# Kernel optimization log

Measured on AMD Instinct MI355X. Metric: run time of the kernel, lower is better.

Reference implementation:

```python
import jax, jax.numpy as jnp
import numpy as np

EPS = 1e-5

def _layernorm(h, g, b):
    m = jnp.mean(h, axis=-1, keepdims=True)
    v = jnp.mean((h - m) ** 2, axis=-1, keepdims=True)
    return (h - m) * jax.lax.rsqrt(v + EPS) * g + b

def setup_inputs() -> dict:
    B, N, D, H, C = 16, 4096, 1024, 512, 2
    key = jax.random.key(0)
    ks = jax.random.split(key, 16)
    def lin(k, fan_in, shape):
        return jax.random.normal(k, shape, dtype=jnp.float32) / np.sqrt(fan_in)
    return {
        "x":   jax.random.normal(ks[0], (B, N, D), dtype=jnp.float32),
        "W1":  lin(ks[1], D, (D, H)),  "b1": jnp.zeros((H,), jnp.float32),
        "g1":  jnp.ones((H,), jnp.float32), "beta1": jnp.zeros((H,), jnp.float32),
        "W2":  lin(ks[2], H, (H, H)),  "b2": jnp.zeros((H,), jnp.float32),
        "g2":  jnp.ones((H,), jnp.float32), "beta2": jnp.zeros((H,), jnp.float32),
        "Wa1": lin(ks[3], H, (H, H)),  "ba1": jnp.zeros((H,), jnp.float32),
        "wa2": lin(ks[4], H, (H, 1)),  "ba2": jnp.zeros((1,), jnp.float32),
        "Wc1": lin(ks[5], H, (H, H)),  "bc1": jnp.zeros((H,), jnp.float32),
        "Wc2": lin(ks[6], H, (H, C)),  "bc2": jnp.zeros((C,), jnp.float32),
    }

def reference(x, W1, b1, g1, beta1, W2, b2, g2, beta2,
              Wa1, ba1, wa2, ba2, Wc1, bc1, Wc2, bc2):
    # Feature extractor: Linear -> LayerNorm -> ReLU (x2); dropout is identity (eval)
    h = jax.nn.relu(_layernorm(jnp.einsum('bnd,dh->bnh', x, W1) + b1, g1, beta1))
    h = jax.nn.relu(_layernorm(jnp.einsum('bnh,hk->bnk', h, W2) + b2, g2, beta2))
    # Attention: Linear -> Tanh -> Linear(->1), softmax over instances (per bag)
    scores = jnp.tanh(jnp.einsum('bnh,hk->bnk', h, Wa1) + ba1) @ wa2 + ba2  # [B,N,1]
    attn = jax.nn.softmax(scores, axis=1)                                   # [B,N,1]
    pooled = jnp.sum(h * attn, axis=1)                                      # [B,H]
    # Classifier (no sample_source path): Linear -> ReLU -> Linear
    logits = jax.nn.relu(pooled @ Wc1 + bc1) @ Wc2 + bc2                    # [B,C]
    return logits
```

## Files before the change

### kernel.cpp

```cpp
#include <hip/hip_runtime.h>
#include <hip/hip_bf16.h>


#define MTOT   65536
#define DDIM   1024
#define HDIM   512
#define NBAG   16
#define NINST  4096

typedef __attribute__((ext_vector_type(8))) short bf16x8;
typedef __attribute__((ext_vector_type(4))) float f32x4;

__device__ __forceinline__ unsigned short f2bf(float f) {
  __hip_bfloat16 h = __float2bfloat16(f);
  unsigned short u;
  __builtin_memcpy(&u, &h, 2);
  return u;
}
__device__ __forceinline__ float bf2f(unsigned short u) {
  unsigned int x = ((unsigned int)u) << 16;
  float f;
  __builtin_memcpy(&f, &x, 4);
  return f;
}

__device__ __forceinline__ void gload16(const void* g, void* l) {
  __builtin_amdgcn_global_load_lds(
      (const __attribute__((address_space(1))) unsigned int*)g,
      (__attribute__((address_space(3))) unsigned int*)l, 16, 0, 0);
}

__device__ __forceinline__ bf16x8 pack8(float4 a, float4 b) {
  bf16x8 r;
  r[0] = (short)f2bf(a.x); r[1] = (short)f2bf(a.y);
  r[2] = (short)f2bf(a.z); r[3] = (short)f2bf(a.w);
  r[4] = (short)f2bf(b.x); r[5] = (short)f2bf(b.y);
  r[6] = (short)f2bf(b.z); r[7] = (short)f2bf(b.w);
  return r;
}

__global__ void transpose_cast(const float* __restrict__ src,
                               __hip_bfloat16* __restrict__ dst,
                               int R, int C) {
  __shared__ float t[32][33];
  const int c0 = blockIdx.x * 32, r0 = blockIdx.y * 32;
  const int tx = threadIdx.x, ty = threadIdx.y;
#pragma unroll
  for (int i = 0; i < 32; i += 8)
    t[ty + i][tx] = src[(size_t)(r0 + ty + i) * C + c0 + tx];
  __syncthreads();
#pragma unroll
  for (int i = 0; i < 32; i += 8)
    dst[(size_t)(c0 + ty + i) * R + r0 + tx] = __float2bfloat16(t[tx][ty + i]);
}

#define BM 128
#define BN 128
#define BK 32

template <int KD, bool AF32, int MODE>
__global__ __launch_bounds__(256, AF32 ? 2 : 3)
void gemm_tile(const void* Ap, const __hip_bfloat16* __restrict__ BT,
               const float* __restrict__ bias,
               __hip_bfloat16* __restrict__ ybuf,
               float2* __restrict__ statp,
               const float* __restrict__ wa2,
               float* __restrict__ scorep) {
  __shared__ __align__(16) char smem[16384];
  __hip_bfloat16* AtP = (__hip_bfloat16*)smem;
  __hip_bfloat16* BtP = (__hip_bfloat16*)(smem + 8192);

  const int tid  = threadIdx.x;
  const int lane = tid & 63;
  const int w    = tid >> 6;
  const int wm   = w >> 1;
  const int wn   = w & 1;
  const int l16  = lane & 15;
  const int lg   = lane >> 4;

  const int cpx = gridDim.x >> 3;
  int bid = blockIdx.x;
  bid = (bid & 7) * cpx + (bid >> 3);
  const int n_blk   = bid & 3;
  const int row_blk = bid >> 2;
  const size_t row0 = (size_t)row_blk * BM;
  const int col0    = n_blk * BN;

  const int rS   = lane & 15;
  const int sS   = (lane >> 4) ^ (lane & 3);
  const int dOff = lane * 8;
  const int frag_off = l16 * 8 + ((lg ^ (l16 & 3)) << 7);

  constexpr int NT = KD / BK;
  const __hip_bfloat16* Abf = (const __hip_bfloat16*)Ap;
  const float* Af32 = (const float*)Ap;

  f32x4 acc[4][4];
#pragma unroll
  for (int i = 0; i < 4; i++)
#pragma unroll
    for (int j = 0; j < 4; j++) acc[i][j] = (f32x4){0.f, 0.f, 0.f, 0.f};

  auto stageB = [&](int kb) {
#pragma unroll
    for (int i = 0; i < 2; i++) {
      const int c = w * 2 + i;
      gload16(BT + (size_t)(col0 + c * 16 + rS) * KD + kb + sS * 8,
              BtP + c * 512 + dOff);
    }
  };
  auto stageA_g = [&](int kb) {
#pragma unroll
    for (int i = 0; i < 2; i++) {
      const int c = w * 2 + i;
      gload16(Abf + (row0 + c * 16 + rS) * KD + kb + sS * 8,
              AtP + c * 512 + dOff);
    }
  };

  float4 f0_0a, f0_0b, f0_1a, f0_1b, f1_0a, f1_0b, f1_1a, f1_1b;
#define LOADA_(S, KB)                                                          \
  { const float* g0_ = Af32 + (row0 + (w * 2 + 0) * 16 + rS) * KD + (KB) + sS * 8; \
    const float* g1_ = Af32 + (row0 + (w * 2 + 1) * 16 + rS) * KD + (KB) + sS * 8; \
    f##S##_0a = *(const float4*)g0_; f##S##_0b = *(const float4*)(g0_ + 4);    \
    f##S##_1a = *(const float4*)g1_; f##S##_1b = *(const float4*)(g1_ + 4); }
#define WRITEA_(S)                                                             \
  { *reinterpret_cast<bf16x8*>(AtP + (w * 2 + 0) * 512 + dOff) =               \
        pack8(f##S##_0a, f##S##_0b);                                           \
    *reinterpret_cast<bf16x8*>(AtP + (w * 2 + 1) * 512 + dOff) =               \
        pack8(f##S##_1a, f##S##_1b); }

#define FRAGS_DECL                                                             \
  bf16x8 af[4], bfr[4];                                                        \
  _Pragma("unroll") for (int fm = 0; fm < 4; fm++)                             \
      af[fm] = *reinterpret_cast<const bf16x8*>(                               \
          AtP + (wm * 4 + fm) * 512 + frag_off);                               \
  _Pragma("unroll") for (int fn = 0; fn < 4; fn++)                             \
      bfr[fn] = *reinterpret_cast<const bf16x8*>(                              \
          BtP + (wn * 4 + fn) * 512 + frag_off);

#define MFMAS                                                                  \
  _Pragma("unroll") for (int fm = 0; fm < 4; fm++)                             \
  _Pragma("unroll") for (int fn = 0; fn < 4; fn++)                             \
      acc[fm][fn] = __builtin_amdgcn_mfma_f32_16x16x32_bf16(                   \
          af[fm], bfr[fn], acc[fm][fn], 0, 0, 0);

  if constexpr (AF32) {
    LOADA_(0, 0);
    for (int tb = 0; tb < NT; tb += 2) {
      {
        WRITEA_(0);
        stageB(tb * BK);
        __syncthreads();
        FRAGS_DECL
        if (tb + 1 < NT) { LOADA_(1, (tb + 1) * BK); }
        MFMAS
        __syncthreads();
      }
      {
        WRITEA_(1);
        stageB((tb + 1) * BK);
        __syncthreads();
        FRAGS_DECL
        if (tb + 2 < NT) { LOADA_(0, (tb + 2) * BK); }
        MFMAS
        __syncthreads();
      }
    }
  } else {
    for (int t = 0; t < NT; ++t) {
      stageA_g(t * BK);
      stageB(t * BK);
      __syncthreads();
      FRAGS_DECL
      MFMAS
      __syncthreads();
    }
  }
#undef LOADA_
#undef WRITEA_
#undef FRAGS_DECL
#undef MFMAS

  float* redS = (float*)smem;
  float* redQ = (float*)smem + 256;

  float biasv[4];
#pragma unroll
  for (int fn = 0; fn < 4; fn++)
    biasv[fn] = bias[col0 + wn * 64 + fn * 16 + l16];

  if (MODE == 0) {
#pragma unroll
    for (int fm = 0; fm < 4; fm++)
#pragma unroll
      for (int r = 0; r < 4; r++) {
        const int rl = wm * 64 + fm * 16 + lg * 4 + r;
        float s1 = 0.f, s2 = 0.f;
#pragma unroll
        for (int fn = 0; fn < 4; fn++) {
          const float z = acc[fm][fn][r] + biasv[fn];
          s1 += z;
          s2 += z * z;
          ybuf[(row0 + rl) * HDIM + col0 + wn * 64 + fn * 16 + l16] =
              __float2bfloat16(z);
        }
#pragma unroll
        for (int m = 1; m < 16; m <<= 1) {
          s1 += __shfl_xor(s1, m);
          s2 += __shfl_xor(s2, m);
        }
        if (l16 == 0) {
          redS[rl * 2 + wn] = s1;
          redQ[rl * 2 + wn] = s2;
        }
      }
    __syncthreads();
    if (tid < BM) {
      statp[(row0 + tid) * 4 + n_blk] =
          make_float2(redS[tid * 2] + redS[tid * 2 + 1],
                      redQ[tid * 2] + redQ[tid * 2 + 1]);
    }
  } else {
    float wv[4];
#pragma unroll
    for (int fn = 0; fn < 4; fn++)
      wv[fn] = wa2[col0 + wn * 64 + fn * 16 + l16];
#pragma unroll
    for (int fm = 0; fm < 4; fm++)
#pragma unroll
      for (int r = 0; r < 4; r++) {
        const int rl = wm * 64 + fm * 16 + lg * 4 + r;
        float s = 0.f;
#pragma unroll
        for (int fn = 0; fn < 4; fn++) {
          const float z = acc[fm][fn][r] + biasv[fn];
          s += tanhf(z) * wv[fn];
        }
#pragma unroll
        for (int m = 1; m < 16; m <<= 1) s += __shfl_xor(s, m);
        if (l16 == 0) redS[rl * 2 + wn] = s;
      }
    __syncthreads();
    if (tid < BM) {
      scorep[(row0 + tid) * 4 + n_blk] = redS[tid * 2] + redS[tid * 2 + 1];
    }
  }
}

__global__ __launch_bounds__(256)
void ln_apply(__hip_bfloat16* __restrict__ y,
              const float2* __restrict__ statp,
              const float* __restrict__ g, const float* __restrict__ be) {
  const int row = blockIdx.x * 4 + (threadIdx.x >> 6);
  const int c0 = (threadIdx.x & 63) * 8;
  const float2* sp = statp + (size_t)row * 4;
  float S = 0.f, Q = 0.f;
#pragma unroll
  for (int j = 0; j < 4; j++) {
    const float2 p = sp[j];
    S += p.x;
    Q += p.y;
  }
  const float mu = S * (1.f / 512.f);
  const float var = Q * (1.f / 512.f) - mu * mu;
  const float rs = rsqrtf(var + 1e-5f);

  __hip_bfloat16* yp = y + (size_t)row * HDIM + c0;
  bf16x8 v = *reinterpret_cast<const bf16x8*>(yp);
  const float4 ga = *(const float4*)(g + c0), gb = *(const float4*)(g + c0 + 4);
  const float4 ba = *(const float4*)(be + c0), bb = *(const float4*)(be + c0 + 4);
  float gv[8] = {ga.x, ga.y, ga.z, ga.w, gb.x, gb.y, gb.z, gb.w};
  float bv[8] = {ba.x, ba.y, ba.z, ba.w, bb.x, bb.y, bb.z, bb.w};
  bf16x8 o;
#pragma unroll
  for (int j = 0; j < 8; j++) {
    const float f = bf2f((unsigned short)v[j]);
    const float h = fmaxf((f - mu) * rs * gv[j] + bv[j], 0.f);
    o[j] = (short)f2bf(h);
  }
  *reinterpret_cast<bf16x8*>(yp) = o;
}

__global__ void softmax_bag(const float* __restrict__ scorep,
                            const float* __restrict__ ba2,
                            float* __restrict__ at) {
  const int b = blockIdx.x;
  const int tid = threadIdx.x;
  const int lane = tid & 63, w = tid >> 6;
  const float bv = ba2[0];
  float v[16];
  float mx = -1e30f;
#pragma unroll
  for (int i = 0; i < 16; i++) {
    const float4 sp = *reinterpret_cast<const float4*>(
        scorep + ((size_t)b * NINST + tid + i * 256) * 4);
    v[i] = sp.x + sp.y + sp.z + sp.w + bv;
    mx = fmaxf(mx, v[i]);
  }
#pragma unroll
  for (int off = 32; off; off >>= 1) mx = fmaxf(mx, __shfl_xor(mx, off));
  __shared__ float red[4];
  if (lane == 0) red[w] = mx;
  __syncthreads();
  mx = fmaxf(fmaxf(red[0], red[1]), fmaxf(red[2], red[3]));
  float sum = 0.f;
#pragma unroll
  for (int i = 0; i < 16; i++) {
    v[i] = expf(v[i] - mx);
    sum += v[i];
  }
#pragma unroll
  for (int off = 32; off; off >>= 1) sum += __shfl_xor(sum, off);
  __shared__ float red2[4];
  if (lane == 0) red2[w] = sum;
  __syncthreads();
  sum = red2[0] + red2[1] + red2[2] + red2[3];
  const float inv = 1.f / sum;
#pragma unroll
  for (int i = 0; i < 16; i++) at[(size_t)b * NINST + tid + i * 256] = v[i] * inv;
}

__global__ void pooled_partial(const __hip_bfloat16* __restrict__ h2,
                               const float* __restrict__ at,
                               float* __restrict__ part) {
  const int bid = blockIdx.x;
  const int b = bid >> 5, cc = (bid >> 3) & 3, nch = bid & 7;
  const int tid = threadIdx.x;
  const int c4 = (tid & 31) * 4, sub = tid >> 5;
  const int n0 = nch * 512;
  const size_t base = (size_t)b * NINST;
  float a0 = 0.f, a1 = 0.f, a2 = 0.f, a3 = 0.f;
  for (int n = n0 + sub; n < n0 + 512; n += 8) {
    const float a = at[base + n];
    const ushort4 u = *reinterpret_cast<const ushort4*>(
        &h2[(base + n) * HDIM + cc * 128 + c4]);
    a0 += a * bf2f(u.x);
    a1 += a * bf2f(u.y);
    a2 += a * bf2f(u.z);
    a3 += a * bf2f(u.w);
  }
  __shared__ float pb[8][128];
  pb[sub][c4 + 0] = a0;
  pb[sub][c4 + 1] = a1;
  pb[sub][c4 + 2] = a2;
  pb[sub][c4 + 3] = a3;
  __syncthreads();
  if (tid < 128) {
    float s = 0.f;
#pragma unroll
    for (int j = 0; j < 8; j++) s += pb[j][tid];
    part[(size_t)nch * 8192 + b * 512 + cc * 128 + tid] = s;
  }
}

__global__ void pooled_reduce(const float* __restrict__ part,
                              float* __restrict__ pooled) {
  const int i = blockIdx.x * 256 + threadIdx.x;
  float s = 0.f;
#pragma unroll
  for (int j = 0; j < 8; j++) s += part[(size_t)j * 8192 + i];
  pooled[i] = s;
}

__global__ void classifier(const float* __restrict__ pooled,
                           const float* __restrict__ Wc1,
                           const float* __restrict__ bc1,
                           const float* __restrict__ Wc2,
                           const float* __restrict__ bc2,
                           float* __restrict__ out) {
  __shared__ float P[NBAG][512];
  __shared__ float Rb[NBAG][512];
  const int tid = threadIdx.x;
#pragma unroll
  for (int i = 0; i < NBAG; i++) P[i][tid] = pooled[i * 512 + tid];
  __syncthreads();
  float r[NBAG];
#pragma unroll
  for (int i = 0; i < NBAG; i++) r[i] = 0.f;
  for (int k = 0; k < 512; k++) {
    const float wv = Wc1[k * 512 + tid];
#pragma unroll
    for (int i = 0; i < NBAG; i++) r[i] += P[i][k] * wv;
  }
#pragma unroll
  for (int i = 0; i < NBAG; i++) Rb[i][tid] = fmaxf(r[i] + bc1[tid], 0.f);
  __syncthreads();
  if (tid < 32) {
    const int i = tid >> 1, c = tid & 1;
    float s = bc2[c];
    for (int k = 0; k < 512; k++) s += Rb[i][k] * Wc2[k * 2 + c];
    out[i * 2 + c] = s;
  }
}

extern "C" void kernel_launch(void* const* d_in, const int* in_sizes, int n_in,
                              void* d_out, int out_size, void* d_ws,
                              size_t ws_size, hipStream_t stream) {
  const float* x   = (const float*)d_in[0];
  const float* W1  = (const float*)d_in[1];
  const float* b1  = (const float*)d_in[2];
  const float* g1  = (const float*)d_in[3];
  const float* be1 = (const float*)d_in[4];
  const float* W2  = (const float*)d_in[5];
  const float* b2  = (const float*)d_in[6];
  const float* g2  = (const float*)d_in[7];
  const float* be2 = (const float*)d_in[8];
  const float* Wa1 = (const float*)d_in[9];
  const float* ba1 = (const float*)d_in[10];
  const float* wa2 = (const float*)d_in[11];
  const float* ba2 = (const float*)d_in[12];
  const float* Wc1 = (const float*)d_in[13];
  const float* bc1 = (const float*)d_in[14];
  const float* Wc2 = (const float*)d_in[15];
  const float* bc2 = (const float*)d_in[16];
  float* out = (float*)d_out;

  char* ws = (char*)d_ws;
  __hip_bfloat16* W1T = (__hip_bfloat16*)(ws + 0);
  __hip_bfloat16* W2T = (__hip_bfloat16*)(ws + 1048576);
  __hip_bfloat16* WaT = (__hip_bfloat16*)(ws + 1572864);
  float2* statp  = (float2*)(ws + 2097152);
  float* scorep  = (float*)(ws + 4194304);
  float* attn    = (float*)(ws + 5242880);
  float* part    = (float*)(ws + 5505024);
  float* pooled  = (float*)(ws + 5767168);
  __hip_bfloat16* buf1 = (__hip_bfloat16*)(ws + 8388608);
  __hip_bfloat16* buf2 = (__hip_bfloat16*)(ws + 75497472);

  transpose_cast<<<dim3(16, 32), dim3(32, 8), 0, stream>>>(W1, W1T, DDIM, HDIM);
  transpose_cast<<<dim3(16, 16), dim3(32, 8), 0, stream>>>(W2, W2T, HDIM, HDIM);
  transpose_cast<<<dim3(16, 16), dim3(32, 8), 0, stream>>>(Wa1, WaT, HDIM, HDIM);

  const int grid = (MTOT / BM) * (HDIM / BN);

  gemm_tile<DDIM, true, 0><<<grid, 256, 0, stream>>>(
      x, W1T, b1, buf1, statp, nullptr, nullptr);
  ln_apply<<<MTOT / 4, 256, 0, stream>>>(buf1, statp, g1, be1);

  gemm_tile<HDIM, false, 0><<<grid, 256, 0, stream>>>(
      buf1, W2T, b2, buf2, statp, nullptr, nullptr);
  ln_apply<<<MTOT / 4, 256, 0, stream>>>(buf2, statp, g2, be2);

  gemm_tile<HDIM, false, 1><<<grid, 256, 0, stream>>>(
      buf2, WaT, ba1, nullptr, nullptr, wa2, scorep);

  softmax_bag<<<NBAG, 256, 0, stream>>>(scorep, ba2, attn);
  pooled_partial<<<512, 256, 0, stream>>>(buf2, attn, part);
  pooled_reduce<<<32, 256, 0, stream>>>(part, pooled);
  classifier<<<1, 512, 0, stream>>>(pooled, Wc1, bc1, Wc2, bc2, out);
}
```

Baseline: 460.0 us.

## Triple-buffer GEMM LDS stages with explicit waitcnt pipelining and MFMA priority

Replaces the single-buffer (bf16 path) and register-double-buffer (fp32 A path) main loops with a three-stage LDS ring, prefetching tiles three K-steps ahead. Waits use explicit vmcnt and lgkmcnt counts and raw barriers instead of __syncthreads, and setprio is raised around the MFMA block. The goal is to hide global-load latency behind the MFMAs. In exchange LDS use grows from 16KB to 48KB per block, which may cut occupancy below the launch-bounds target, and the hand-counted vmcnt values must match the number of outstanding loads.

```diff
diff --git a/kernel.cpp b/kernel.cpp
--- a/kernel.cpp
+++ b/kernel.cpp
@@ -38,6 +38,11 @@
   r[6] = (short)f2bf(b.z); r[7] = (short)f2bf(b.w);
   return r;
 }
+
+#define VMW(N)  asm volatile("s_waitcnt vmcnt(" #N ")" ::: "memory")
+#define LKW0    asm volatile("s_waitcnt lgkmcnt(0)" ::: "memory")
+#define SB0     __builtin_amdgcn_sched_barrier(0)
+#define BARRIER __builtin_amdgcn_s_barrier()
 
 __global__ void transpose_cast(const float* __restrict__ src,
                                __hip_bfloat16* __restrict__ dst,
@@ -66,9 +71,7 @@
                float2* __restrict__ statp,
                const float* __restrict__ wa2,
                float* __restrict__ scorep) {
-  __shared__ __align__(16) char smem[16384];
-  __hip_bfloat16* AtP = (__hip_bfloat16*)smem;
-  __hip_bfloat16* BtP = (__hip_bfloat16*)(smem + 8192);
+  __shared__ __align__(16) char smem[49152];
 
   const int tid  = threadIdx.x;
   const int lane = tid & 63;
@@ -101,87 +104,134 @@
 #pragma unroll
     for (int j = 0; j < 4; j++) acc[i][j] = (f32x4){0.f, 0.f, 0.f, 0.f};
 
-  auto stageB = [&](int kb) {
+  auto stageB = [&](int kb, int j) {
 #pragma unroll
     for (int i = 0; i < 2; i++) {
       const int c = w * 2 + i;
       gload16(BT + (size_t)(col0 + c * 16 + rS) * KD + kb + sS * 8,
-              BtP + c * 512 + dOff);
+              (__hip_bfloat16*)(smem + j * 16384 + 8192) + c * 512 + dOff);
     }
   };
-  auto stageA_g = [&](int kb) {
+  auto stageA = [&](int kb, int j) {
 #pragma unroll
     for (int i = 0; i < 2; i++) {
       const int c = w * 2 + i;
       gload16(Abf + (row0 + c * 16 + rS) * KD + kb + sS * 8,
-              AtP + c * 512 + dOff);
+              (__hip_bfloat16*)(smem + j * 16384) + c * 512 + dOff);
     }
   };
 
-  float4 f0_0a, f0_0b, f0_1a, f0_1b, f1_0a, f1_0b, f1_1a, f1_1b;
-#define LOADA_(S, KB)                                                          \
-  { const float* g0_ = Af32 + (row0 + (w * 2 + 0) * 16 + rS) * KD + (KB) + sS * 8; \
-    const float* g1_ = Af32 + (row0 + (w * 2 + 1) * 16 + rS) * KD + (KB) + sS * 8; \
-    f##S##_0a = *(const float4*)g0_; f##S##_0b = *(const float4*)(g0_ + 4);    \
-    f##S##_1a = *(const float4*)g1_; f##S##_1b = *(const float4*)(g1_ + 4); }
-#define WRITEA_(S)                                                             \
-  { *reinterpret_cast<bf16x8*>(AtP + (w * 2 + 0) * 512 + dOff) =               \
-        pack8(f##S##_0a, f##S##_0b);                                           \
-    *reinterpret_cast<bf16x8*>(AtP + (w * 2 + 1) * 512 + dOff) =               \
-        pack8(f##S##_1a, f##S##_1b); }
-
-#define FRAGS_DECL                                                             \
-  bf16x8 af[4], bfr[4];                                                        \
-  _Pragma("unroll") for (int fm = 0; fm < 4; fm++)                             \
-      af[fm] = *reinterpret_cast<const bf16x8*>(                               \
-          AtP + (wm * 4 + fm) * 512 + frag_off);                               \
-  _Pragma("unroll") for (int fn = 0; fn < 4; fn++)                             \
-      bfr[fn] = *reinterpret_cast<const bf16x8*>(                              \
-          BtP + (wn * 4 + fn) * 512 + frag_off);
-
-#define MFMAS                                                                  \
-  _Pragma("unroll") for (int fm = 0; fm < 4; fm++)                             \
-  _Pragma("unroll") for (int fn = 0; fn < 4; fn++)                             \
-      acc[fm][fn] = __builtin_amdgcn_mfma_f32_16x16x32_bf16(                   \
-          af[fm], bfr[fn], acc[fm][fn], 0, 0, 0);
+#define LOADA_(SET, KB)                                                        \
+  _Pragma("unroll") for (int i_ = 0; i_ < 2; i_++) {                           \
+    const float* gp_ =                                                         \
+        Af32 + (row0 + (w * 2 + i_) * 16 + rS) * KD + (KB) + sS * 8;           \
+    SET[i_ * 2 + 0] = *(const float4*)gp_;                                     \
+    SET[i_ * 2 + 1] = *(const float4*)(gp_ + 4);                               \
+  }
+#define CVTW_(SET, J)                                                          \
+  _Pragma("unroll") for (int i_ = 0; i_ < 2; i_++)                             \
+    *reinterpret_cast<bf16x8*>((__hip_bfloat16*)(smem + (J) * 16384) +         \
+                               (w * 2 + i_) * 512 + dOff) =                    \
+        pack8(SET[i_ * 2 + 0], SET[i_ * 2 + 1]);
+
+#define FRAGS_(J)                                                              \
+  _Pragma("unroll") for (int f_ = 0; f_ < 4; f_++)                             \
+      af[f_] = *reinterpret_cast<const bf16x8*>(                               \
+          (__hip_bfloat16*)(smem + (J) * 16384) + (wm * 4 + f_) * 512 +        \
+          frag_off);                                                           \
+  _Pragma("unroll") for (int f_ = 0; f_ < 4; f_++)                             \
+      bfr[f_] = *reinterpret_cast<const bf16x8*>(                              \
+          (__hip_bfloat16*)(smem + (J) * 16384 + 8192) + (wn * 4 + f_) * 512 + \
+          frag_off);
+
+#define MFMAS_                                                                 \
+  _Pragma("unroll") for (int fm_ = 0; fm_ < 4; fm_++)                          \
+  _Pragma("unroll") for (int fn_ = 0; fn_ < 4; fn_++)                          \
+      acc[fm_][fn_] = __builtin_amdgcn_mfma_f32_16x16x32_bf16(                 \
+          af[fm_], bfr[fn_], acc[fm_][fn_], 0, 0, 0);
+
+#define STEP_G(J, T, VMN)                                                      \
+  {                                                                            \
+    VMW(VMN);                                                                  \
+    BARRIER;                                                                   \
+    bf16x8 af[4], bfr[4];                                                      \
+    FRAGS_(J);                                                                 \
+    LKW0; SB0;                                                                 \
+    BARRIER;                                                                   \
+    if ((T) + 3 < NT) {                                                        \
+      stageA(((T) + 3) * BK, (J));                                             \
+      stageB(((T) + 3) * BK, (J));                                             \
+    }                                                                          \
+    __builtin_amdgcn_s_setprio(1);                                             \
+    MFMAS_;                                                                    \
+    __builtin_amdgcn_s_setprio(0);                                             \
+  }
+
+#define STEP_F(J, T, VMN)                                                      \
+  {                                                                            \
+    VMW(VMN);                                                                  \
+    CVTW_(set##J, (J));                                                        \
+    LKW0;                                                                      \
+    BARRIER;                                                                   \
+    bf16x8 af[4], bfr[4];                                                      \
+    FRAGS_(J);                                                                 \
+    LKW0; SB0;                                                                 \
+    BARRIER;                                                                   \
+    if ((T) + 3 < NT) {                                                        \
+      LOADA_(set##J, ((T) + 3) * BK);                                          \
+      stageB(((T) + 3) * BK, (J));                                             \
+    }                                                                          \
+    __builtin_amdgcn_s_setprio(1);                                             \
+    MFMAS_;                                                                    \
+    __builtin_amdgcn_s_setprio(0);                                             \
+  }
 
   if constexpr (AF32) {
-    LOADA_(0, 0);
-    for (int tb = 0; tb < NT; tb += 2) {
-      {
-        WRITEA_(0);
-        stageB(tb * BK);
-        __syncthreads();
-        FRAGS_DECL
-        if (tb + 1 < NT) { LOADA_(1, (tb + 1) * BK); }
-        MFMAS
-        __syncthreads();
-      }
-      {
-        WRITEA_(1);
-        stageB((tb + 1) * BK);
-        __syncthreads();
-        FRAGS_DECL
-        if (tb + 2 < NT) { LOADA_(0, (tb + 2) * BK); }
-        MFMAS
-        __syncthreads();
-      }
+    float4 set0[4], set1[4], set2[4];
+    LOADA_(set0, 0);       stageB(0, 0);
+    LOADA_(set1, BK);      stageB(BK, 1);
+    LOADA_(set2, 2 * BK);  stageB(2 * BK, 2);
+    for (int tb = 0; tb + 5 <= NT; tb += 3) {
+      STEP_F(0, tb, 12)
+      STEP_F(1, tb + 1, 12)
+      STEP_F(2, tb + 2, 12)
+    }
+    if constexpr (NT % 3 == 1) {
+      STEP_F(0, NT - 4, 12)
+      STEP_F(1, NT - 3, 12)
+      STEP_F(2, NT - 2, 6)
+      STEP_F(0, NT - 1, 0)
+    } else {
+      STEP_F(0, NT - 2, 6)
+      STEP_F(1, NT - 1, 0)
     }
   } else {
-    for (int t = 0; t < NT; ++t) {
-      stageA_g(t * BK);
-      stageB(t * BK);
-      __syncthreads();
-      FRAGS_DECL
-      MFMAS
-      __syncthreads();
-    }
-  }
+    stageA(0, 0);       stageB(0, 0);
+    stageA(BK, 1);      stageB(BK, 1);
+    stageA(2 * BK, 2);  stageB(2 * BK, 2);
+    for (int tb = 0; tb + 5 <= NT; tb += 3) {
+      STEP_G(0, tb, 8)
+      STEP_G(1, tb + 1, 8)
+      STEP_G(2, tb + 2, 8)
+    }
+    if constexpr (NT % 3 == 1) {
+      STEP_G(0, NT - 4, 8)
+      STEP_G(1, NT - 3, 8)
+      STEP_G(2, NT - 2, 4)
+      STEP_G(0, NT - 1, 0)
+    } else {
+      STEP_G(0, NT - 2, 4)
+      STEP_G(1, NT - 1, 0)
+    }
+  }
+#undef STEP_G
+#undef STEP_F
 #undef LOADA_
-#undef WRITEA_
-#undef FRAGS_DECL
-#undef MFMAS
-
+#undef CVTW_
+#undef FRAGS_
+#undef MFMAS_
+
+  __syncthreads();
   float* redS = (float*)smem;
   float* redQ = (float*)smem + 256;
 
```

Result: no change. 458.4 us (-0.3%).
